# Performance work log

Measured on AMD Instinct MI355X. Metric: run time of the kernel, lower is better.

The kernel has to match this reference:

```python
import jax, jax.numpy as jnp
import numpy as np

H = 2048  # hidden_size
B, S = 4, 4096
LEVELS = 3  # hierarchical_compression_levels


def _linear_params(key, out_dim, in_dim):
    kw, kb = jax.random.split(key)
    bound = 1.0 / np.sqrt(in_dim)
    W = jax.random.uniform(kw, (out_dim, in_dim), minval=-bound, maxval=bound, dtype=jnp.float32)
    b = jax.random.uniform(kb, (out_dim,), minval=-bound, maxval=bound, dtype=jnp.float32)
    return W, b


def setup_inputs() -> dict:
    key = jax.random.key(0)
    ks = jax.random.split(key, 12)
    inp = {}
    inp['hidden_states'] = jax.random.normal(ks[0], (B, S, H), dtype=jnp.float32)
    inp['access_frequency'] = jax.random.uniform(ks[1], (B, S), dtype=jnp.float32)
    inp['importance_score'] = jax.random.uniform(ks[2], (B, S), dtype=jnp.float32)
    # compression level 1: H -> H/2 -> H/2 -> H ; level 2: H -> H/4 -> H/4 -> H
    inp['comp1_W'], inp['comp1_b'] = _linear_params(ks[3], H // 2, H)
    inp['adapt1_W'], inp['adapt1_b'] = _linear_params(ks[4], H // 2, H // 2)
    inp['decomp1_W'], inp['decomp1_b'] = _linear_params(ks[5], H, H // 2)
    inp['comp2_W'], inp['comp2_b'] = _linear_params(ks[6], H // 4, H)
    inp['adapt2_W'], inp['adapt2_b'] = _linear_params(ks[7], H // 4, H // 4)
    inp['decomp2_W'], inp['decomp2_b'] = _linear_params(ks[8], H, H // 4)
    # strategy selector: Linear(H, H/4) -> ReLU -> Linear(H/4, LEVELS) -> Softmax
    inp['sel1_W'], inp['sel1_b'] = _linear_params(ks[9], H // 4, H)
    inp['sel2_W'], inp['sel2_b'] = _linear_params(ks[10], LEVELS, H // 4)
    return inp


def reference(hidden_states, access_frequency, importance_score,
              comp1_W, comp1_b, adapt1_W, adapt1_b, decomp1_W, decomp1_b,
              comp2_W, comp2_b, adapt2_W, adapt2_b, decomp2_W, decomp2_b,
              sel1_W, sel1_b, sel2_W, sel2_b):
    h = hidden_states
    h2 = h.shape[-1] // 2
    # _get_compression_strategy: scale first half by freq, second half by importance
    combined = jnp.concatenate(
        [h[..., :h2] * access_frequency[..., None],
         h[..., h2:] * importance_score[..., None]], axis=-1)  # [B,S,H]
    hid = jax.nn.relu(jnp.einsum('bsh,oh->bso', combined, sel1_W) + sel1_b)
    strategy_weights = jax.nn.softmax(jnp.einsum('bso,lo->bsl', hid, sel2_W) + sel2_b, axis=-1)
    selected = jnp.argmax(strategy_weights, axis=-1)  # [B,S] int

    def branch(Wc, bc, Wa, ba, Wd, bd):
        c = jnp.einsum('bsh,oh->bso', h, Wc) + bc          # compress
        c = jnp.einsum('bso,po->bsp', c, Wa) + ba          # frequency adaptor
        return jnp.einsum('bsp,hp->bsh', c, Wd) + bd       # decompress

    out1 = branch(comp1_W, comp1_b, adapt1_W, adapt1_b, decomp1_W, decomp1_b)
    out2 = branch(comp2_W, comp2_b, adapt2_W, adapt2_b, decomp2_W, decomp2_b)
    stacked = jnp.stack([h, out1, out2], axis=2)  # [B,S,LEVELS,H]
    compressed = jnp.take_along_axis(stacked, selected[:, :, None, None], axis=2)[:, :, 0, :]
    return compressed
```

## Files before the change

kernel.cpp:

```cpp
#include <hip/hip_runtime.h>
#include <hip/hip_bf16.h>

#define TOK 16384
#define TAU2 0.001f
#define CFENCE asm volatile("" ::: "memory")

typedef __attribute__((ext_vector_type(8))) short short8;
typedef __attribute__((ext_vector_type(4))) float f32x4;

__device__ __forceinline__ unsigned short f32_bf16(float f) {
  __hip_bfloat16 h = __float2bfloat16(f);
  unsigned short u;
  __builtin_memcpy(&u, &h, sizeof(u));
  return u;
}
__device__ __forceinline__ float bf16_f32(unsigned short u) {
  union { unsigned int i; float f; } c; c.i = ((unsigned int)u) << 16; return c.f;
}

__device__ __forceinline__ void gll16(const unsigned short* g, unsigned short* l) {
  __builtin_amdgcn_global_load_lds(
      (const __attribute__((address_space(1))) unsigned int*)g,
      (__attribute__((address_space(3))) unsigned int*)l, 16, 0, 0);
}

__global__ void zero3(int* a, int* c) {
  if (threadIdx.x == 0) { *a = 0; c[0] = 0; c[1] = 0; }
}

__global__ void cvt_kernel(const float* __restrict__ s, unsigned short* __restrict__ d, int n4) {
  int i = blockIdx.x * 256 + threadIdx.x;
  if (i < n4) {
    float4 v = ((const float4*)s)[i];
    union { unsigned short u[4]; uint2 q; } pk;
    pk.u[0] = f32_bf16(v.x); pk.u[1] = f32_bf16(v.y);
    pk.u[2] = f32_bf16(v.z); pk.u[3] = f32_bf16(v.w);
    ((uint2*)d)[i] = pk.q;
  }
}

__global__ void cvt_split_kernel(const float* __restrict__ s,
                                 unsigned short* __restrict__ dhi,
                                 unsigned short* __restrict__ dlo, int n4) {
  int i = blockIdx.x * 256 + threadIdx.x;
  if (i < n4) {
    float4 v = ((const float4*)s)[i];
    const float* f = (const float*)&v;
    union { unsigned short u[4]; uint2 q; } hi, lo;
    #pragma unroll
    for (int e = 0; e < 4; e++) {
      unsigned short h = f32_bf16(f[e]);
      hi.u[e] = h;
      lo.u[e] = f32_bf16(f[e] - bf16_f32(h));
    }
    ((uint2*)dhi)[i] = hi.q;
    ((uint2*)dlo)[i] = lo.q;
  }
}

__global__ void compact_sel(const int* __restrict__ sel, int* __restrict__ idx1,
                            int* __restrict__ idx2, int* __restrict__ cnt) {
  int t = blockIdx.x * 256 + threadIdx.x;
  int s = sel[t];
  if (s == 1) idx1[atomicAdd(&cnt[0], 1)] = t;
  else if (s == 2) idx2[atomicAdd(&cnt[1], 1)] = t;
}

__global__ void pad_idx(int* __restrict__ idx1, int* __restrict__ idx2,
                        const int* __restrict__ cnt, int* __restrict__ mc) {
  const int tid = threadIdx.x;
  const int n1 = cnt[0], n2 = cnt[1];
  const int p1 = (n1 + 127) & ~(int)127, p2 = (n2 + 127) & ~(int)127;
  if (tid < p1 - n1) idx1[n1 + tid] = -1;
  if (tid < p2 - n2) idx2[n2 + tid] = -1;
  if (tid == 0) { mc[0] = p1; mc[1] = p2; }
}

#define XCD_DECODE(LOG2NC)                                                    \
  const int wgid = blockIdx.x;                                                \
  const int xcd = wgid & 7;                                                   \
  const int slot = wgid >> 3;                                                 \
  const int n0 = (slot & ((1 << (LOG2NC)) - 1)) * 128;                        \
  const int m0 = ((slot >> (LOG2NC)) * 8 + xcd) * 128;

template<int EPI, int AG, int LOG2NC>
__device__ __forceinline__
void gemm_body(const unsigned short* __restrict__ A,
               const unsigned short* __restrict__ Bw,
               const float* __restrict__ bias,
               void* __restrict__ Outv,
               const int* __restrict__ idx, const int* __restrict__ mcp,
               int N, int K) {
  __shared__ __align__(16) unsigned short As[3 * 128 * 32];
  __shared__ __align__(16) unsigned short Bs[3 * 128 * 32];
  const int tid = threadIdx.x;
  XCD_DECODE(LOG2NC)
  if (mcp && m0 >= *mcp) return;
  const int lane = tid & 63, wave = tid >> 6;
  const int wm = wave >> 1, wn = wave & 1;
  const int quad = lane >> 4, lr = lane & 15;

  const int srow = tid >> 2;
  const int schunk = (tid & 3) ^ (srow & 3);
  unsigned int aoff[2], boff[2];
  #pragma unroll
  for (int r = 0; r < 2; r++) {
    int row = r * 64 + srow;
    int gr = m0 + row;
    if (AG) { int t = idx[gr]; gr = (t < 0) ? 0 : t; }
    aoff[r] = (unsigned int)gr * (unsigned int)K + (unsigned int)(schunk * 8);
    boff[r] = (unsigned int)(n0 + row) * (unsigned int)K + (unsigned int)(schunk * 8);
  }
  const int lds_dst = tid * 8;

  f32x4 acc[4][4] = {};
  const int nk = K >> 5;

  #define STAGE(T, O)                                                        \
    {                                                                        \
      const unsigned int k0 = (unsigned int)(T) << 5;                        \
      gll16(A + aoff[0] + k0, &As[(O) + lds_dst]);                           \
      gll16(A + aoff[1] + k0, &As[(O) + 2048 + lds_dst]);                    \
      gll16(Bw + boff[0] + k0, &Bs[(O) + lds_dst]);                          \
      gll16(Bw + boff[1] + k0, &Bs[(O) + 2048 + lds_dst]);                   \
    }
  #define COMPUTE(O)                                                         \
    {                                                                        \
      short8 af[4], bfr[4];                                                  \
      _Pragma("unroll")                                                      \
      for (int i = 0; i < 4; i++) {                                          \
        const int row = wm * 64 + i * 16 + lr;                               \
        af[i] = *(const short8*)(&As[(O) + row * 32 + ((quad ^ (row & 3)) << 3)]); \
      }                                                                      \
      _Pragma("unroll")                                                      \
      for (int j = 0; j < 4; j++) {                                          \
        const int row = wn * 64 + j * 16 + lr;                               \
        bfr[j] = *(const short8*)(&Bs[(O) + row * 32 + ((quad ^ (row & 3)) << 3)]); \
      }                                                                      \
      _Pragma("unroll")                                                      \
      for (int i = 0; i < 4; i++)                                            \
        _Pragma("unroll")                                                    \
        for (int j = 0; j < 4; j++)                                          \
          acc[i][j] = __builtin_amdgcn_mfma_f32_16x16x32_bf16(af[i], bfr[j], acc[i][j], 0, 0, 0); \
    }

  int oA = 0, oB = 4096, oC = 8192;
  STAGE(0, oA);
  STAGE(1, oB);

  for (int t = 0; t < nk - 2; t++) {
    STAGE(t + 2, oC);
    asm volatile("s_waitcnt vmcnt(8)" ::: "memory");
    CFENCE; __builtin_amdgcn_s_barrier(); CFENCE;
    COMPUTE(oA);
    CFENCE; __builtin_amdgcn_s_barrier(); CFENCE;
    int tmp = oA; oA = oB; oB = oC; oC = tmp;
  }
  asm volatile("s_waitcnt vmcnt(4)" ::: "memory");
  CFENCE; __builtin_amdgcn_s_barrier(); CFENCE;
  COMPUTE(oA);
  CFENCE; __builtin_amdgcn_s_barrier(); CFENCE;
  { int tmp = oA; oA = oB; oB = oC; oC = tmp; }
  asm volatile("s_waitcnt vmcnt(0)" ::: "memory");
  CFENCE; __builtin_amdgcn_s_barrier(); CFENCE;
  COMPUTE(oA);
  #undef STAGE
  #undef COMPUTE

  #pragma unroll
  for (int i = 0; i < 4; i++) {
    const int rbase = m0 + wm * 64 + i * 16 + quad * 4;
    #pragma unroll
    for (int j = 0; j < 4; j++) {
      const int col = n0 + wn * 64 + j * 16 + lr;
      const float bv = bias[col];
      #pragma unroll
      for (int r = 0; r < 4; r++) {
        const int row = rbase + r;
        float v = acc[i][j][r] + bv;
        if (EPI == 0) {
          ((unsigned short*)Outv)[(size_t)row * N + col] = f32_bf16(v);
        } else {
          const int tk = idx[row];
          if (tk >= 0) ((float*)Outv)[(size_t)tk * N + col] = v;
        }
      }
    }
  }
}

#define GEMM_SHELL(NAME, EPI, AG, LOG2NC)                                      \
__global__ __launch_bounds__(256, 3) void NAME(                                \
    const unsigned short* __restrict__ A,                                      \
    const unsigned short* __restrict__ Bw,                                     \
    const float* __restrict__ bias, void* __restrict__ Outv,                   \
    const int* __restrict__ idx, const int* __restrict__ mcp, int N, int K) {  \
  gemm_body<EPI, AG, LOG2NC>(A, Bw, bias, Outv, idx, mcp, N, K);               \
}
GEMM_SHELL(g_comp1, 0, 1, 3)
GEMM_SHELL(g_comp2, 0, 1, 2)
GEMM_SHELL(g_adapt1, 0, 0, 3)
GEMM_SHELL(g_adapt2, 0, 0, 2)
GEMM_SHELL(g_dec1, 4, 0, 4)
GEMM_SHELL(g_dec2, 4, 0, 4)

__global__ __launch_bounds__(256, 2)
void gemm_sel(const float* __restrict__ Af,
              const unsigned short* __restrict__ Bw,
              const unsigned short* __restrict__ Bw2,
              const float* __restrict__ bias,
              float* __restrict__ Out,
              const float* __restrict__ scA, const float* __restrict__ scB,
              int N, int K) {
  __shared__ __align__(16) unsigned short As[2 * 128 * 32];
  __shared__ __align__(16) unsigned short Bs[2 * 128 * 32];
  const int LO = 128 * 32;
  const int tid = threadIdx.x;
  XCD_DECODE(2)
  const int lane = tid & 63, wave = tid >> 6;
  const int wm = wave >> 1, wn = wave & 1;
  const int quad = lane >> 4, lr = lane & 15;
  const int srow = tid >> 1, scol = (tid & 1) * 16;

  const size_t aRowOff = (size_t)(m0 + srow) * K;
  const unsigned short* Brow = Bw + (size_t)(n0 + srow) * K;
  const unsigned short* Brow2 = Bw2 + (size_t)(n0 + srow) * K;

  f32x4 acc[4][4] = {};

  for (int k0 = 0; k0 < K; k0 += 32) {
    {
      const float4* src = (const float4*)(Af + aRowOff + k0 + scol);
      float4 f[4];
      f[0] = src[0]; f[1] = src[1]; f[2] = src[2]; f[3] = src[3];
      const int tk = m0 + srow;
      const float s = ((k0 + scol) * 2 < K) ? scA[tk] : scB[tk];
      union { unsigned short u[16]; uint4 q[2]; } hi;
      union { unsigned short u[16]; uint4 q[2]; } lo;
      const float* ff = (const float*)f;
      #pragma unroll
      for (int e = 0; e < 16; e++) {
        float fv = ff[e] * s;
        unsigned short hb = f32_bf16(fv);
        hi.u[e] = hb;
        lo.u[e] = f32_bf16(fv - bf16_f32(hb));
      }
      uint4* dst = (uint4*)(As + srow * 32 + scol);
      dst[0] = hi.q[0]; dst[1] = hi.q[1];
      uint4* dst2 = (uint4*)(As + LO + srow * 32 + scol);
      dst2[0] = lo.q[0]; dst2[1] = lo.q[1];
    }
    {
      const uint4* src = (const uint4*)(Brow + k0 + scol);
      uint4* dst = (uint4*)(Bs + srow * 32 + scol);
      dst[0] = src[0]; dst[1] = src[1];
      const uint4* src2 = (const uint4*)(Brow2 + k0 + scol);
      uint4* dst2 = (uint4*)(Bs + LO + srow * 32 + scol);
      dst2[0] = src2[0]; dst2[1] = src2[1];
    }
    __syncthreads();
    short8 af[4], bfr[4], af2[4], bf2[4];
    #pragma unroll
    for (int i = 0; i < 4; i++) {
      af[i]  = *(const short8*)(As + (wm * 64 + i * 16 + lr) * 32 + quad * 8);
      af2[i] = *(const short8*)(As + LO + (wm * 64 + i * 16 + lr) * 32 + quad * 8);
    }
    #pragma unroll
    for (int j = 0; j < 4; j++) {
      bfr[j] = *(const short8*)(Bs + (wn * 64 + j * 16 + lr) * 32 + quad * 8);
      bf2[j] = *(const short8*)(Bs + LO + (wn * 64 + j * 16 + lr) * 32 + quad * 8);
    }
    #pragma unroll
    for (int i = 0; i < 4; i++)
      #pragma unroll
      for (int j = 0; j < 4; j++) {
        acc[i][j] = __builtin_amdgcn_mfma_f32_16x16x32_bf16(af[i], bfr[j], acc[i][j], 0, 0, 0);
        acc[i][j] = __builtin_amdgcn_mfma_f32_16x16x32_bf16(af[i], bf2[j], acc[i][j], 0, 0, 0);
        acc[i][j] = __builtin_amdgcn_mfma_f32_16x16x32_bf16(af2[i], bfr[j], acc[i][j], 0, 0, 0);
      }
    __syncthreads();
  }

  #pragma unroll
  for (int i = 0; i < 4; i++) {
    const int rbase = m0 + wm * 64 + i * 16 + quad * 4;
    #pragma unroll
    for (int j = 0; j < 4; j++) {
      const int col = n0 + wn * 64 + j * 16 + lr;
      const float bv = bias[col];
      #pragma unroll
      for (int r = 0; r < 4; r++) {
        const int row = rbase + r;
        float v = acc[i][j][r] + bv;
        Out[(size_t)row * N + col] = fmaxf(v, 0.0f);
      }
    }
  }
}

__global__ __launch_bounds__(256)
void selector_logits_f32(const float* __restrict__ hidf,
                         const float* __restrict__ W2, const float* __restrict__ b2,
                         int* __restrict__ sel, int* __restrict__ risky,
                         int* __restrict__ riskyCount) {
  const int wave = threadIdx.x >> 6, lane = threadIdx.x & 63;
  const int token = blockIdx.x * 4 + wave;
  const float* hs = hidf + (size_t)token * 512 + lane * 8;
  float4 h0 = *(const float4*)hs, h1 = *(const float4*)(hs + 4);
  float p[3];
  #pragma unroll
  for (int c = 0; c < 3; c++) {
    const float* w = W2 + c * 512 + lane * 8;
    float4 w0 = *(const float4*)w, w1 = *(const float4*)(w + 4);
    p[c] = h0.x*w0.x + h0.y*w0.y + h0.z*w0.z + h0.w*w0.w
         + h1.x*w1.x + h1.y*w1.y + h1.z*w1.z + h1.w*w1.w;
  }
  #pragma unroll
  for (int off = 32; off >= 1; off >>= 1) {
    #pragma unroll
    for (int c = 0; c < 3; c++) p[c] += __shfl_xor(p[c], off, 64);
  }
  if (lane == 0) {
    float l0 = p[0] + b2[0], l1 = p[1] + b2[1], l2 = p[2] + b2[2];
    int arg = 0; float best = l0;
    if (l1 > best) { best = l1; arg = 1; }
    if (l2 > best) { best = l2; arg = 2; }
    float second;
    if (arg == 0) second = fmaxf(l1, l2);
    else if (arg == 1) second = fmaxf(l0, l2);
    else second = fmaxf(l0, l1);
    sel[token] = arg;
    if (best - second < TAU2) {
      int idx = atomicAdd(riskyCount, 1);
      risky[idx] = token;
    }
  }
}

__global__ __launch_bounds__(256)
void recheck_exact(const float* __restrict__ h, const float* __restrict__ freq,
                   const float* __restrict__ imp,
                   const float* __restrict__ W1, const float* __restrict__ b1,
                   const float* __restrict__ W2, const float* __restrict__ b2,
                   const int* __restrict__ risky, const int* __restrict__ riskyCount,
                   int* __restrict__ sel) {
  __shared__ float h_sh[2048];
  __shared__ float hid_sh[512];
  const int n = *riskyCount;
  const int tid = threadIdx.x;
  for (int ri = blockIdx.x; ri < n; ri += gridDim.x) {
    const int token = risky[ri];
    {
      const float s = (tid < 128) ? freq[token] : imp[token];
      const float4* src = (const float4*)(h + (size_t)token * 2048) + tid * 2;
      float4 v0 = src[0], v1 = src[1];
      v0.x *= s; v0.y *= s; v0.z *= s; v0.w *= s;
      v1.x *= s; v1.y *= s; v1.z *= s; v1.w *= s;
      ((float4*)h_sh)[tid * 2] = v0;
      ((float4*)h_sh)[tid * 2 + 1] = v1;
    }
    __syncthreads();
    #pragma unroll
    for (int half = 0; half < 2; half++) {
      const int o = tid + half * 256;
      const float* wrow = W1 + (size_t)o * 2048;
      float a0 = 0.f, a1 = 0.f, a2 = 0.f, a3 = 0.f;
      for (int k = 0; k < 2048; k += 16) {
        float4 w0 = *(const float4*)(wrow + k);
        float4 w1v = *(const float4*)(wrow + k + 4);
        float4 w2v = *(const float4*)(wrow + k + 8);
        float4 w3v = *(const float4*)(wrow + k + 12);
        float4 x0 = *(const float4*)(h_sh + k);
        float4 x1 = *(const float4*)(h_sh + k + 4);
        float4 x2 = *(const float4*)(h_sh + k + 8);
        float4 x3 = *(const float4*)(h_sh + k + 12);
        a0 += w0.x*x0.x + w0.y*x0.y + w0.z*x0.z + w0.w*x0.w;
        a1 += w1v.x*x1.x + w1v.y*x1.y + w1v.z*x1.z + w1v.w*x1.w;
        a2 += w2v.x*x2.x + w2v.y*x2.y + w2v.z*x2.z + w2v.w*x2.w;
        a3 += w3v.x*x3.x + w3v.y*x3.y + w3v.z*x3.z + w3v.w*x3.w;
      }
      hid_sh[o] = fmaxf((a0 + a1) + (a2 + a3) + b1[o], 0.0f);
    }
    __syncthreads();
    if (tid < 64) {
      const int lane = tid;
      const float* hs = &hid_sh[lane * 8];
      float l[3];
      #pragma unroll
      for (int c = 0; c < 3; c++) {
        const float* w = W2 + c * 512 + lane * 8;
        float s = 0.0f;
        #pragma unroll
        for (int e = 0; e < 8; e++) s += hs[e] * w[e];
        l[c] = s;
      }
      #pragma unroll
      for (int off = 32; off >= 1; off >>= 1)
        #pragma unroll
        for (int c = 0; c < 3; c++) l[c] += __shfl_xor(l[c], off, 64);
      if (lane == 0) {
        float l0 = l[0] + b2[0], l1 = l[1] + b2[1], l2 = l[2] + b2[2];
        int arg = 0; float best = l0;
        if (l1 > best) { best = l1; arg = 1; }
        if (l2 > best) { arg = 2; }
        sel[token] = arg;
      }
    }
    __syncthreads();
  }
}

__global__ __launch_bounds__(256)
void copy_sel0(const float* __restrict__ h, const int* __restrict__ sel,
               float* __restrict__ out) {
  for (int token = blockIdx.x; token < TOK; token += gridDim.x) {
    if (sel[token] != 0) continue;
    const float4* src = (const float4*)(h + (size_t)token * 2048);
    float4* dst = (float4*)(out + (size_t)token * 2048);
    dst[threadIdx.x] = src[threadIdx.x];
    dst[threadIdx.x + 256] = src[threadIdx.x + 256];
  }
}

extern "C" void kernel_launch(void* const* d_in, const int* in_sizes, int n_in,
                              void* d_out, int out_size, void* d_ws, size_t ws_size,
                              hipStream_t stream) {
  const float* h        = (const float*)d_in[0];
  const float* freq     = (const float*)d_in[1];
  const float* imp      = (const float*)d_in[2];
  const float* comp1W   = (const float*)d_in[3];
  const float* comp1b   = (const float*)d_in[4];
  const float* adapt1W  = (const float*)d_in[5];
  const float* adapt1b  = (const float*)d_in[6];
  const float* decomp1W = (const float*)d_in[7];
  const float* decomp1b = (const float*)d_in[8];
  const float* comp2W   = (const float*)d_in[9];
  const float* comp2b   = (const float*)d_in[10];
  const float* adapt2W  = (const float*)d_in[11];
  const float* adapt2b  = (const float*)d_in[12];
  const float* decomp2W = (const float*)d_in[13];
  const float* decomp2b = (const float*)d_in[14];
  const float* sel1W    = (const float*)d_in[15];
  const float* sel1b    = (const float*)d_in[16];
  const float* sel2W    = (const float*)d_in[17];
  const float* sel2b    = (const float*)d_in[18];
  float* out = (float*)d_out;

  char* ws = (char*)d_ws;
  size_t off = 0;
  auto alloc = [&](size_t bytes) -> void* {
    void* p = ws + off; off += (bytes + 255) & ~(size_t)255; return p;
  };
  unsigned short* wb_comp1   = (unsigned short*)alloc((size_t)1024 * 2048 * 2);
  unsigned short* wb_adapt1  = (unsigned short*)alloc((size_t)1024 * 1024 * 2);
  unsigned short* wb_decomp1 = (unsigned short*)alloc((size_t)2048 * 1024 * 2);
  unsigned short* wb_comp2   = (unsigned short*)alloc((size_t)512 * 2048 * 2);
  unsigned short* wb_adapt2  = (unsigned short*)alloc((size_t)512 * 512 * 2);
  unsigned short* wb_decomp2 = (unsigned short*)alloc((size_t)2048 * 512 * 2);
  unsigned short* w1hi       = (unsigned short*)alloc((size_t)512 * 2048 * 2);
  unsigned short* w1lo       = (unsigned short*)alloc((size_t)512 * 2048 * 2);
  float*          hidf       = (float*)alloc((size_t)TOK * 512 * 4);
  unsigned short* c1         = (unsigned short*)alloc((size_t)TOK * 1024 * 2);
  unsigned short* a1         = (unsigned short*)alloc((size_t)TOK * 1024 * 2);
  int* sel        = (int*)alloc((size_t)TOK * 4);
  int* risky      = (int*)alloc((size_t)TOK * 4);
  int* riskyCount = (int*)alloc(256);
  int* idx1       = (int*)alloc((size_t)TOK * 4);
  int* idx2       = (int*)alloc((size_t)TOK * 4);
  int* cnt        = (int*)alloc(256);
  int* mc         = (int*)alloc(256);

  unsigned short* hb = (unsigned short*)out;
  unsigned short* c2 = (unsigned short*)hidf;
  unsigned short* a2 = (unsigned short*)hidf + (size_t)TOK * 512;

  zero3<<<1, 64, 0, stream>>>(riskyCount, cnt);

  auto cvt = [&](const float* s, unsigned short* d, int n) {
    cvt_kernel<<<(n / 4 + 255) / 256, 256, 0, stream>>>(s, d, n / 4);
  };
  cvt(comp1W,   wb_comp1,   1024 * 2048);
  cvt(adapt1W,  wb_adapt1,  1024 * 1024);
  cvt(decomp1W, wb_decomp1, 2048 * 1024);
  cvt(comp2W,   wb_comp2,   512 * 2048);
  cvt(adapt2W,  wb_adapt2,  512 * 512);
  cvt(decomp2W, wb_decomp2, 2048 * 512);
  cvt(h,        hb,         TOK * 2048);
  cvt_split_kernel<<<(512 * 2048 / 4 + 255) / 256, 256, 0, stream>>>(
      sel1W, w1hi, w1lo, 512 * 2048 / 4);

  gemm_sel<<<4 * 128, 256, 0, stream>>>(
      h, w1hi, w1lo, sel1b, hidf, freq, imp, 512, 2048);
  selector_logits_f32<<<TOK / 4, 256, 0, stream>>>(hidf, sel2W, sel2b, sel, risky, riskyCount);
  recheck_exact<<<256, 256, 0, stream>>>(h, freq, imp, sel1W, sel1b, sel2W, sel2b,
                                         risky, riskyCount, sel);

  compact_sel<<<TOK / 256, 256, 0, stream>>>(sel, idx1, idx2, cnt);
  pad_idx<<<1, 256, 0, stream>>>(idx1, idx2, cnt, mc);

  g_comp1<<<8 * 128, 256, 0, stream>>>(
      hb, wb_comp1, comp1b, c1, idx1, mc + 0, 1024, 2048);
  g_comp2<<<4 * 128, 256, 0, stream>>>(
      hb, wb_comp2, comp2b, c2, idx2, mc + 1, 512, 2048);
  g_adapt1<<<8 * 128, 256, 0, stream>>>(
      c1, wb_adapt1, adapt1b, a1, nullptr, mc + 0, 1024, 1024);
  g_adapt2<<<4 * 128, 256, 0, stream>>>(
      c2, wb_adapt2, adapt2b, a2, nullptr, mc + 1, 512, 512);
  g_dec1<<<16 * 128, 256, 0, stream>>>(
      a1, wb_decomp1, decomp1b, out, idx1, mc + 0, 2048, 1024);
  g_dec2<<<16 * 128, 256, 0, stream>>>(
      a2, wb_decomp2, decomp2b, out, idx2, mc + 1, 2048, 512);

  copy_sel0<<<2048, 256, 0, stream>>>(h, sel, out);
}
```

Measured before the change: 893.0 us.

## Factor selector scaling out of GEMM and use plain bf16 pipelined GEMMs

The per-token frequency and importance scales are constant across each half of K, so they are pulled out of the selector GEMM. It becomes two single-bf16 half-K GEMMs on the already converted hidden states, using the pipelined gemm_body with new leading-dimension parameters. The scaling, bias and ReLU are applied in the logits kernel. This drops the hi/lo split GEMM with its triple MFMA and per-tile fp32 conversion. The precision loss is covered by widening the risky-margin threshold TAU2 from 0.001 to 0.02, which sends more tokens to the exact recheck.

```diff
diff --git a/kernel.cpp b/kernel.cpp
--- a/kernel.cpp
+++ b/kernel.cpp
@@ -2,7 +2,7 @@
 #include <hip/hip_bf16.h>
 
 #define TOK 16384
-#define TAU2 0.001f
+#define TAU2 0.02f
 #define CFENCE asm volatile("" ::: "memory")
 
 typedef __attribute__((ext_vector_type(8))) short short8;
@@ -39,25 +39,6 @@
   }
 }
 
-__global__ void cvt_split_kernel(const float* __restrict__ s,
-                                 unsigned short* __restrict__ dhi,
-                                 unsigned short* __restrict__ dlo, int n4) {
-  int i = blockIdx.x * 256 + threadIdx.x;
-  if (i < n4) {
-    float4 v = ((const float4*)s)[i];
-    const float* f = (const float*)&v;
-    union { unsigned short u[4]; uint2 q; } hi, lo;
-    #pragma unroll
-    for (int e = 0; e < 4; e++) {
-      unsigned short h = f32_bf16(f[e]);
-      hi.u[e] = h;
-      lo.u[e] = f32_bf16(f[e] - bf16_f32(h));
-    }
-    ((uint2*)dhi)[i] = hi.q;
-    ((uint2*)dlo)[i] = lo.q;
-  }
-}
-
 __global__ void compact_sel(const int* __restrict__ sel, int* __restrict__ idx1,
                             int* __restrict__ idx2, int* __restrict__ cnt) {
   int t = blockIdx.x * 256 + threadIdx.x;
@@ -90,7 +71,7 @@
                const float* __restrict__ bias,
                void* __restrict__ Outv,
                const int* __restrict__ idx, const int* __restrict__ mcp,
-               int N, int K) {
+               int N, int K, int LDA, int LDB) {
   __shared__ __align__(16) unsigned short As[3 * 128 * 32];
   __shared__ __align__(16) unsigned short Bs[3 * 128 * 32];
   const int tid = threadIdx.x;
@@ -108,8 +89,8 @@
     int row = r * 64 + srow;
     int gr = m0 + row;
     if (AG) { int t = idx[gr]; gr = (t < 0) ? 0 : t; }
-    aoff[r] = (unsigned int)gr * (unsigned int)K + (unsigned int)(schunk * 8);
-    boff[r] = (unsigned int)(n0 + row) * (unsigned int)K + (unsigned int)(schunk * 8);
+    aoff[r] = (unsigned int)gr * (unsigned int)LDA + (unsigned int)(schunk * 8);
+    boff[r] = (unsigned int)(n0 + row) * (unsigned int)LDB + (unsigned int)(schunk * 8);
   }
   const int lds_dst = tid * 8;
 
@@ -173,16 +154,18 @@
     #pragma unroll
     for (int j = 0; j < 4; j++) {
       const int col = n0 + wn * 64 + j * 16 + lr;
-      const float bv = bias[col];
+      const float bv = (EPI == 5) ? 0.0f : bias[col];
       #pragma unroll
       for (int r = 0; r < 4; r++) {
         const int row = rbase + r;
         float v = acc[i][j][r] + bv;
         if (EPI == 0) {
           ((unsigned short*)Outv)[(size_t)row * N + col] = f32_bf16(v);
-        } else {
+        } else if (EPI == 4) {
           const int tk = idx[row];
           if (tk >= 0) ((float*)Outv)[(size_t)tk * N + col] = v;
+        } else {
+          ((float*)Outv)[(size_t)row * N + col] = v;
         }
       }
     }
@@ -194,8 +177,9 @@
     const unsigned short* __restrict__ A,                                      \
     const unsigned short* __restrict__ Bw,                                     \
     const float* __restrict__ bias, void* __restrict__ Outv,                   \
-    const int* __restrict__ idx, const int* __restrict__ mcp, int N, int K) {  \
-  gemm_body<EPI, AG, LOG2NC>(A, Bw, bias, Outv, idx, mcp, N, K);               \
+    const int* __restrict__ idx, const int* __restrict__ mcp,                  \
+    int N, int K, int LDA, int LDB) {                                          \
+  gemm_body<EPI, AG, LOG2NC>(A, Bw, bias, Outv, idx, mcp, N, K, LDA, LDB);     \
 }
 GEMM_SHELL(g_comp1, 0, 1, 3)
 GEMM_SHELL(g_comp2, 0, 1, 2)
@@ -203,117 +187,41 @@
 GEMM_SHELL(g_adapt2, 0, 0, 2)
 GEMM_SHELL(g_dec1, 4, 0, 4)
 GEMM_SHELL(g_dec2, 4, 0, 4)
-
-__global__ __launch_bounds__(256, 2)
-void gemm_sel(const float* __restrict__ Af,
-              const unsigned short* __restrict__ Bw,
-              const unsigned short* __restrict__ Bw2,
-              const float* __restrict__ bias,
-              float* __restrict__ Out,
-              const float* __restrict__ scA, const float* __restrict__ scB,
-              int N, int K) {
-  __shared__ __align__(16) unsigned short As[2 * 128 * 32];
-  __shared__ __align__(16) unsigned short Bs[2 * 128 * 32];
-  const int LO = 128 * 32;
-  const int tid = threadIdx.x;
-  XCD_DECODE(2)
-  const int lane = tid & 63, wave = tid >> 6;
-  const int wm = wave >> 1, wn = wave & 1;
-  const int quad = lane >> 4, lr = lane & 15;
-  const int srow = tid >> 1, scol = (tid & 1) * 16;
-
-  const size_t aRowOff = (size_t)(m0 + srow) * K;
-  const unsigned short* Brow = Bw + (size_t)(n0 + srow) * K;
-  const unsigned short* Brow2 = Bw2 + (size_t)(n0 + srow) * K;
-
-  f32x4 acc[4][4] = {};
-
-  for (int k0 = 0; k0 < K; k0 += 32) {
-    {
-      const float4* src = (const float4*)(Af + aRowOff + k0 + scol);
-      float4 f[4];
-      f[0] = src[0]; f[1] = src[1]; f[2] = src[2]; f[3] = src[3];
-      const int tk = m0 + srow;
-      const float s = ((k0 + scol) * 2 < K) ? scA[tk] : scB[tk];
-      union { unsigned short u[16]; uint4 q[2]; } hi;
-      union { unsigned short u[16]; uint4 q[2]; } lo;
-      const float* ff = (const float*)f;
-      #pragma unroll
-      for (int e = 0; e < 16; e++) {
-        float fv = ff[e] * s;
-        unsigned short hb = f32_bf16(fv);
-        hi.u[e] = hb;
-        lo.u[e] = f32_bf16(fv - bf16_f32(hb));
-      }
-      uint4* dst = (uint4*)(As + srow * 32 + scol);
-      dst[0] = hi.q[0]; dst[1] = hi.q[1];
-      uint4* dst2 = (uint4*)(As + LO + srow * 32 + scol);
-      dst2[0] = lo.q[0]; dst2[1] = lo.q[1];
-    }
-    {
-      const uint4* src = (const uint4*)(Brow + k0 + scol);
-      uint4* dst = (uint4*)(Bs + srow * 32 + scol);
-      dst[0] = src[0]; dst[1] = src[1];
-      const uint4* src2 = (const uint4*)(Brow2 + k0 + scol);
-      uint4* dst2 = (uint4*)(Bs + LO + srow * 32 + scol);
-      dst2[0] = src2[0]; dst2[1] = src2[1];
-    }
-    __syncthreads();
-    short8 af[4], bfr[4], af2[4], bf2[4];
-    #pragma unroll
-    for (int i = 0; i < 4; i++) {
-      af[i]  = *(const short8*)(As + (wm * 64 + i * 16 + lr) * 32 + quad * 8);
-      af2[i] = *(const short8*)(As + LO + (wm * 64 + i * 16 + lr) * 32 + quad * 8);
-    }
-    #pragma unroll
-    for (int j = 0; j < 4; j++) {
-      bfr[j] = *(const short8*)(Bs + (wn * 64 + j * 16 + lr) * 32 + quad * 8);
-      bf2[j] = *(const short8*)(Bs + LO + (wn * 64 + j * 16 + lr) * 32 + quad * 8);
-    }
-    #pragma unroll
-    for (int i = 0; i < 4; i++)
-      #pragma unroll
-      for (int j = 0; j < 4; j++) {
-        acc[i][j] = __builtin_amdgcn_mfma_f32_16x16x32_bf16(af[i], bfr[j], acc[i][j], 0, 0, 0);
-        acc[i][j] = __builtin_amdgcn_mfma_f32_16x16x32_bf16(af[i], bf2[j], acc[i][j], 0, 0, 0);
-        acc[i][j] = __builtin_amdgcn_mfma_f32_16x16x32_bf16(af2[i], bfr[j], acc[i][j], 0, 0, 0);
-      }
-    __syncthreads();
-  }
-
-  #pragma unroll
-  for (int i = 0; i < 4; i++) {
-    const int rbase = m0 + wm * 64 + i * 16 + quad * 4;
-    #pragma unroll
-    for (int j = 0; j < 4; j++) {
-      const int col = n0 + wn * 64 + j * 16 + lr;
-      const float bv = bias[col];
-      #pragma unroll
-      for (int r = 0; r < 4; r++) {
-        const int row = rbase + r;
-        float v = acc[i][j][r] + bv;
-        Out[(size_t)row * N + col] = fmaxf(v, 0.0f);
-      }
-    }
-  }
-}
+GEMM_SHELL(g_sel1a, 5, 0, 2)
+GEMM_SHELL(g_sel1b, 5, 0, 2)
 
 __global__ __launch_bounds__(256)
-void selector_logits_f32(const float* __restrict__ hidf,
-                         const float* __restrict__ W2, const float* __restrict__ b2,
-                         int* __restrict__ sel, int* __restrict__ risky,
-                         int* __restrict__ riskyCount) {
+void selector_logits2(const float* __restrict__ G1, const float* __restrict__ G2,
+                      const float* __restrict__ freq, const float* __restrict__ imp,
+                      const float* __restrict__ b1,
+                      const float* __restrict__ W2, const float* __restrict__ b2,
+                      int* __restrict__ sel, int* __restrict__ risky,
+                      int* __restrict__ riskyCount) {
   const int wave = threadIdx.x >> 6, lane = threadIdx.x & 63;
   const int token = blockIdx.x * 4 + wave;
-  const float* hs = hidf + (size_t)token * 512 + lane * 8;
-  float4 h0 = *(const float4*)hs, h1 = *(const float4*)(hs + 4);
+  const float fq = freq[token], im = imp[token];
+  const float* g1 = G1 + (size_t)token * 512 + lane * 8;
+  const float* g2 = G2 + (size_t)token * 512 + lane * 8;
+  const float* bb = b1 + lane * 8;
+  float4 a0 = *(const float4*)g1, a1 = *(const float4*)(g1 + 4);
+  float4 c0 = *(const float4*)g2, c1 = *(const float4*)(g2 + 4);
+  float4 bl0 = *(const float4*)bb, bl1 = *(const float4*)(bb + 4);
+  float hid[8];
+  hid[0] = fmaxf(fq * a0.x + im * c0.x + bl0.x, 0.f);
+  hid[1] = fmaxf(fq * a0.y + im * c0.y + bl0.y, 0.f);
+  hid[2] = fmaxf(fq * a0.z + im * c0.z + bl0.z, 0.f);
+  hid[3] = fmaxf(fq * a0.w + im * c0.w + bl0.w, 0.f);
+  hid[4] = fmaxf(fq * a1.x + im * c1.x + bl1.x, 0.f);
+  hid[5] = fmaxf(fq * a1.y + im * c1.y + bl1.y, 0.f);
+  hid[6] = fmaxf(fq * a1.z + im * c1.z + bl1.z, 0.f);
+  hid[7] = fmaxf(fq * a1.w + im * c1.w + bl1.w, 0.f);
   float p[3];
   #pragma unroll
   for (int c = 0; c < 3; c++) {
     const float* w = W2 + c * 512 + lane * 8;
     float4 w0 = *(const float4*)w, w1 = *(const float4*)(w + 4);
-    p[c] = h0.x*w0.x + h0.y*w0.y + h0.z*w0.z + h0.w*w0.w
-         + h1.x*w1.x + h1.y*w1.y + h1.z*w1.z + h1.w*w1.w;
+    p[c] = hid[0]*w0.x + hid[1]*w0.y + hid[2]*w0.z + hid[3]*w0.w
+         + hid[4]*w1.x + hid[5]*w1.y + hid[6]*w1.z + hid[7]*w1.w;
   }
   #pragma unroll
   for (int off = 32; off >= 1; off >>= 1) {
@@ -457,8 +365,7 @@
   unsigned short* wb_comp2   = (unsigned short*)alloc((size_t)512 * 2048 * 2);
   unsigned short* wb_adapt2  = (unsigned short*)alloc((size_t)512 * 512 * 2);
   unsigned short* wb_decomp2 = (unsigned short*)alloc((size_t)2048 * 512 * 2);
-  unsigned short* w1hi       = (unsigned short*)alloc((size_t)512 * 2048 * 2);
-  unsigned short* w1lo       = (unsigned short*)alloc((size_t)512 * 2048 * 2);
+  unsigned short* wb_sel1    = (unsigned short*)alloc((size_t)512 * 2048 * 2);
   float*          hidf       = (float*)alloc((size_t)TOK * 512 * 4);
   unsigned short* c1         = (unsigned short*)alloc((size_t)TOK * 1024 * 2);
   unsigned short* a1         = (unsigned short*)alloc((size_t)TOK * 1024 * 2);
@@ -471,6 +378,7 @@
   int* mc         = (int*)alloc(256);
 
   unsigned short* hb = (unsigned short*)out;
+  float* G2 = out + (size_t)16 * 1024 * 1024;
   unsigned short* c2 = (unsigned short*)hidf;
   unsigned short* a2 = (unsigned short*)hidf + (size_t)TOK * 512;
 
@@ -485,13 +393,15 @@
   cvt(comp2W,   wb_comp2,   512 * 2048);
   cvt(adapt2W,  wb_adapt2,  512 * 512);
   cvt(decomp2W, wb_decomp2, 2048 * 512);
+  cvt(sel1W,    wb_sel1,    512 * 2048);
   cvt(h,        hb,         TOK * 2048);
-  cvt_split_kernel<<<(512 * 2048 / 4 + 255) / 256, 256, 0, stream>>>(
-      sel1W, w1hi, w1lo, 512 * 2048 / 4);
-
-  gemm_sel<<<4 * 128, 256, 0, stream>>>(
-      h, w1hi, w1lo, sel1b, hidf, freq, imp, 512, 2048);
-  selector_logits_f32<<<TOK / 4, 256, 0, stream>>>(hidf, sel2W, sel2b, sel, risky, riskyCount);
+
+  g_sel1a<<<4 * 128, 256, 0, stream>>>(
+      hb, wb_sel1, nullptr, hidf, nullptr, nullptr, 512, 1024, 2048, 2048);
+  g_sel1b<<<4 * 128, 256, 0, stream>>>(
+      hb + 1024, wb_sel1 + 1024, nullptr, G2, nullptr, nullptr, 512, 1024, 2048, 2048);
+  selector_logits2<<<TOK / 4, 256, 0, stream>>>(
+      hidf, G2, freq, imp, sel1b, sel2W, sel2b, sel, risky, riskyCount);
   recheck_exact<<<256, 256, 0, stream>>>(h, freq, imp, sel1W, sel1b, sel2W, sel2b,
                                          risky, riskyCount, sel);
 
@@ -499,17 +409,17 @@
   pad_idx<<<1, 256, 0, stream>>>(idx1, idx2, cnt, mc);
 
   g_comp1<<<8 * 128, 256, 0, stream>>>(
-      hb, wb_comp1, comp1b, c1, idx1, mc + 0, 1024, 2048);
+      hb, wb_comp1, comp1b, c1, idx1, mc + 0, 1024, 2048, 2048, 2048);
   g_comp2<<<4 * 128, 256, 0, stream>>>(
-      hb, wb_comp2, comp2b, c2, idx2, mc + 1, 512, 2048);
+      hb, wb_comp2, comp2b, c2, idx2, mc + 1, 512, 2048, 2048, 2048);
   g_adapt1<<<8 * 128, 256, 0, stream>>>(
-      c1, wb_adapt1, adapt1b, a1, nullptr, mc + 0, 1024, 1024);
+      c1, wb_adapt1, adapt1b, a1, nullptr, mc + 0, 1024, 1024, 1024, 1024);
   g_adapt2<<<4 * 128, 256, 0, stream>>>(
-      c2, wb_adapt2, adapt2b, a2, nullptr, mc + 1, 512, 512);
+      c2, wb_adapt2, adapt2b, a2, nullptr, mc + 1, 512, 512, 512, 512);
   g_dec1<<<16 * 128, 256, 0, stream>>>(
-      a1, wb_decomp1, decomp1b, out, idx1, mc + 0, 2048, 1024);
+      a1, wb_decomp1, decomp1b, out, idx1, mc + 0, 2048, 1024, 1024, 1024);
   g_dec2<<<16 * 128, 256, 0, stream>>>(
-      a2, wb_decomp2, decomp2b, out, idx2, mc + 1, 2048, 512);
+      a2, wb_decomp2, decomp2b, out, idx2, mc + 1, 2048, 512, 512, 512);
 
   copy_sel0<<<2048, 256, 0, stream>>>(h, sel, out);
 }
```

Measured after the change: 2.181 ms. 144% more time.
